# Kernel optimization log

Measured on AMD Instinct MI355X. Metric: run time of the kernel, lower is better.

## Reference

```python
import jax, jax.numpy as jnp
import numpy as np

N_NODES = 40000
N_EDGES = 640000
D_IN = 128
D_HID = 128
D_OUT = 128
N_GRAPHS = 128


def setup_inputs() -> dict:
    key = jax.random.key(0)
    ks = jax.random.split(key, 12)
    x = jax.random.normal(ks[0], (N_NODES, D_IN), dtype=jnp.float32)
    edge_index = jax.random.randint(ks[1], (2, N_EDGES), 0, N_NODES, dtype=jnp.int64)
    batch = jnp.sort(jax.random.randint(ks[2], (N_NODES,), 0, N_GRAPHS, dtype=jnp.int64))
    def lin(k, fan_in, shape):
        s = 1.0 / np.sqrt(fan_in)
        return jax.random.uniform(k, shape, dtype=jnp.float32, minval=-s, maxval=s)
    return {
        "x": x, "edge_index": edge_index, "batch": batch,
        "W_rel0": lin(ks[3], D_IN, (D_IN, D_HID)), "b_rel0": lin(ks[4], D_IN, (D_HID,)), "W_root0": lin(ks[5], D_IN, (D_IN, D_HID)),
        "W_rel1": lin(ks[6], D_HID, (D_HID, D_HID)), "b_rel1": lin(ks[7], D_HID, (D_HID,)), "W_root1": lin(ks[8], D_HID, (D_HID, D_HID)),
        "W_rel2": lin(ks[9], D_HID, (D_HID, D_OUT)), "b_rel2": lin(ks[10], D_HID, (D_OUT,)), "W_root2": lin(ks[11], D_HID, (D_HID, D_OUT)),
    }


def graph_conv(x, src, dst, W_rel, b_rel, W_root):
    # PyG GraphConv: out_i = Lin_rel(sum_{j in N(i)} x_j) + Lin_root(x_i)
    agg = jax.ops.segment_sum(x[src], dst, num_segments=N_NODES)  # [N, F]
    return agg @ W_rel + b_rel + x @ W_root


def reference(x, edge_index, batch,
              W_rel0, b_rel0, W_root0,
              W_rel1, b_rel1, W_root1,
              W_rel2, b_rel2, W_root2):
    src, dst = edge_index[0], edge_index[1]
    h = graph_conv(x, src, dst, W_rel0, b_rel0, W_root0)
    h = jax.nn.relu(h)  # dropout is identity in eval mode
    h = graph_conv(h, src, dst, W_rel1, b_rel1, W_root1)
    h = jax.nn.relu(h)
    h = graph_conv(h, src, dst, W_rel2, b_rel2, W_root2)
    # global_max_pool over per-node graph ids -> [n_graphs, D_OUT]
    return jax.ops.segment_max(h, batch, num_segments=N_GRAPHS)
```

## Files before the change

kernel.cpp:

```cpp
#include <hip/hip_runtime.h>
#include <hip/hip_bf16.h>
#include <math.h>

#define N_NODES 40000
#define N_EDGES 640000
#define D 128
#define N_GRAPHS 128
#define SCAN_NBLK ((N_NODES + 255) / 256)
#define LDS_STRIDE 68

typedef __attribute__((ext_vector_type(8))) short bf16x8;
typedef __attribute__((ext_vector_type(4))) float f32x4;
typedef __attribute__((ext_vector_type(4))) unsigned int u32x4;

static __device__ __forceinline__ unsigned short f2b(float f) {
    unsigned int u = __float_as_uint(f);
    unsigned int r = (u + 0x7fffu + ((u >> 16) & 1u)) >> 16;
    return (unsigned short)r;
}
static __device__ __forceinline__ float blo(unsigned int u) {
    return __uint_as_float(u << 16);
}
static __device__ __forceinline__ float bhi(unsigned int u) {
    return __uint_as_float(u & 0xffff0000u);
}
static __device__ __forceinline__ unsigned int fkey(float x) {
    unsigned int b = __float_as_uint(x);
    return (b & 0x80000000u) ? ~b : (b | 0x80000000u);
}

__global__ void __launch_bounds__(256) k_init(
    int* __restrict__ counts,
    unsigned short* __restrict__ xb, unsigned short* __restrict__ hA,
    unsigned short* __restrict__ hB, unsigned int* __restrict__ outk) {
    int n = blockIdx.x * 256 + threadIdx.x;
    if (n < N_GRAPHS * D) outk[n] = 0x007FFFFFu;
    if (n < N_NODES) counts[n] = 0;
    if (blockIdx.x == SCAN_NBLK) {
        int t = threadIdx.x;
        if (t < 48) {
            int row = t >> 4, c = t & 15;
            unsigned short* p = (row == 0) ? xb : (row == 1) ? hA : hB;
            u32x4 z = {0u, 0u, 0u, 0u};
            ((u32x4*)(p + (size_t)N_NODES * D))[c] = z;
        }
    }
}

__global__ void __launch_bounds__(256) k_pack1(
    const int* __restrict__ ei, int* __restrict__ counts,
    const float* __restrict__ x, unsigned int* __restrict__ xb,
    const float* __restrict__ Wr0, const float* __restrict__ Wt0,
    const float* __restrict__ Wr1, const float* __restrict__ Wt1,
    const float* __restrict__ Wr2, const float* __restrict__ Wt2,
    unsigned short* __restrict__ WT) {
    int b = blockIdx.x;
    int t = threadIdx.x;
    if (b < 2500) {
        int e = b * 256 + t;
        atomicAdd(&counts[ei[N_EDGES + e]], 1);
    } else if (b < 5000) {
        int i = (b - 2500) * 256 + t;
        const f32x4* xv = (const f32x4*)x;
        f32x4 v0 = xv[i * 2], v1 = xv[i * 2 + 1];
        u32x4 o;
        o.x = ((unsigned int)f2b(v0.y) << 16) | f2b(v0.x);
        o.y = ((unsigned int)f2b(v0.w) << 16) | f2b(v0.z);
        o.z = ((unsigned int)f2b(v1.y) << 16) | f2b(v1.x);
        o.w = ((unsigned int)f2b(v1.w) << 16) | f2b(v1.z);
        ((u32x4*)xb)[i] = o;
    } else {
        int bw = b - 5000;
        int l = bw >> 7, c = bw & 127, k = t;
        const float* Wrel = (l == 0) ? Wr0 : (l == 1) ? Wr1 : Wr2;
        const float* Wroot = (l == 0) ? Wt0 : (l == 1) ? Wt1 : Wt2;
        float v = (k < D) ? Wrel[k * D + c] : Wroot[(k - D) * D + c];
        WT[(size_t)l * 128 * 256 + c * 256 + k] = f2b(v);
    }
}

__global__ void __launch_bounds__(256) k_scan1(const int* __restrict__ counts,
                                               int* __restrict__ local_pre,
                                               int* __restrict__ blocksums) {
    int t = threadIdx.x;
    int i = blockIdx.x * 256 + t;
    int lane = t & 63, wave = t >> 6;
    int v = (i < N_NODES) ? ((counts[i] + 15) & ~15) : 0;
    int incl = v;
#pragma unroll
    for (int off = 1; off < 64; off <<= 1) {
        int u = __shfl_up(incl, off);
        if (lane >= off) incl += u;
    }
    __shared__ int ws[4];
    if (lane == 63) ws[wave] = incl;
    __syncthreads();
    int base = 0;
    for (int w = 0; w < 4; ++w) {
        int s = ws[w];
        if (w < wave) base += s;
    }
    if (i < N_NODES) local_pre[i] = base + incl - v;
    if (t == 255) blocksums[blockIdx.x] = base + incl;
}

__global__ void __launch_bounds__(256) k_scan3(const int* __restrict__ local_pre,
                                               const int* __restrict__ blocksums,
                                               const int* __restrict__ counts,
                                               int* __restrict__ rp_pad,
                                               int* __restrict__ cursor,
                                               int* __restrict__ src_pad) {
    int t = threadIdx.x;
    int lane = t & 63, wave = t >> 6;
    int bid = blockIdx.x;
    int v = (t < bid) ? blocksums[t] : 0;
#pragma unroll
    for (int off = 32; off >= 1; off >>= 1) v += __shfl_xor(v, off);
    __shared__ int ws[4];
    if (lane == 0) ws[wave] = v;
    __syncthreads();
    int base = ws[0] + ws[1] + ws[2] + ws[3];

    int i = bid * 256 + t;
    if (i < N_NODES) {
        int rp = base + local_pre[i];
        rp_pad[i] = rp;
        cursor[i] = rp;
        int c = counts[i];
        int pc = (c + 15) & ~15;
        for (int j = rp + c; j < rp + pc; ++j) src_pad[j] = N_NODES;
        if (i == N_NODES - 1) rp_pad[N_NODES] = rp + pc;
    }
}

__global__ void k_scatter(const int* __restrict__ ei, int* __restrict__ cursor,
                          int* __restrict__ src_pad) {
    int e = blockIdx.x * blockDim.x + threadIdx.x;
    if (e < N_EDGES) {
        int d = ei[N_EDGES + e];
        int pos = atomicAdd(&cursor[d], 1);
        src_pad[pos] = ei[e];
    }
}

__global__ void __launch_bounds__(256) k_layer(
    const unsigned short* __restrict__ in,
    const int* __restrict__ rp_pad,
    const int* __restrict__ src_pad,
    const unsigned short* __restrict__ WT,
    const float* __restrict__ bias,
    unsigned short* __restrict__ out,
    const int* __restrict__ batch,
    unsigned int* __restrict__ outk) {
    __shared__ unsigned int aggLDS[16 * LDS_STRIDE];
    int tid = threadIdx.x;
    int w = tid >> 6;
    int lane = tid & 63;
    int q = lane >> 4;
    int c = lane & 15;
    int nl = w * 4 + q;
    int nodebase = blockIdx.x * 16;
    const u32x4* inv = (const u32x4*)in;

    int s = rp_pad[nodebase + nl];
    int e = rp_pad[nodebase + nl + 1];
    const int4* sidx = (const int4*)(src_pad + s);
    int ntrips = (e - s) >> 4;

    float a0 = 0.f, a1 = 0.f, a2 = 0.f, a3 = 0.f;
    float a4 = 0.f, a5 = 0.f, a6 = 0.f, a7 = 0.f;

#define ACC8(v) do { \
        a0 += blo((v).x); a1 += bhi((v).x); \
        a2 += blo((v).y); a3 += bhi((v).y); \
        a4 += blo((v).z); a5 += bhi((v).z); \
        a6 += blo((v).w); a7 += bhi((v).w); } while (0)

    for (int t = 0; t < ntrips; ++t) {
        int4 ia = sidx[4 * t + 0];
        int4 ib = sidx[4 * t + 1];
        int4 ic = sidx[4 * t + 2];
        int4 id = sidx[4 * t + 3];
        u32x4 v0 = inv[ia.x * 16 + c];
        u32x4 v1 = inv[ia.y * 16 + c];
        u32x4 v2 = inv[ia.z * 16 + c];
        u32x4 v3 = inv[ia.w * 16 + c];
        u32x4 v4 = inv[ib.x * 16 + c];
        u32x4 v5 = inv[ib.y * 16 + c];
        u32x4 v6 = inv[ib.z * 16 + c];
        u32x4 v7 = inv[ib.w * 16 + c];
        u32x4 v8 = inv[ic.x * 16 + c];
        u32x4 v9 = inv[ic.y * 16 + c];
        u32x4 va = inv[ic.z * 16 + c];
        u32x4 vb = inv[ic.w * 16 + c];
        u32x4 vc = inv[id.x * 16 + c];
        u32x4 vd = inv[id.y * 16 + c];
        u32x4 ve = inv[id.z * 16 + c];
        u32x4 vf = inv[id.w * 16 + c];
        ACC8(v0); ACC8(v1); ACC8(v2); ACC8(v3);
        ACC8(v4); ACC8(v5); ACC8(v6); ACC8(v7);
        ACC8(v8); ACC8(v9); ACC8(va); ACC8(vb);
        ACC8(vc); ACC8(vd); ACC8(ve); ACC8(vf);
    }
#undef ACC8

    u32x4 o;
    o.x = ((unsigned int)f2b(a1) << 16) | f2b(a0);
    o.y = ((unsigned int)f2b(a3) << 16) | f2b(a2);
    o.z = ((unsigned int)f2b(a5) << 16) | f2b(a4);
    o.w = ((unsigned int)f2b(a7) << 16) | f2b(a6);
    *(u32x4*)&aggLDS[nl * LDS_STRIDE + c * 4] = o;
    __syncthreads();

    int row = c, quad = q;
    int colbase = w * 32;

    f32x4 acc0 = {0.f, 0.f, 0.f, 0.f};
    f32x4 acc1 = {0.f, 0.f, 0.f, 0.f};

    const unsigned int* Al = &aggLDS[row * LDS_STRIDE];
    const short* Xp = (const short*)(in + (nodebase + row) * D);
    const short* W0 = (const short*)(WT + (colbase + row) * 256);
    const short* W1 = (const short*)(WT + (colbase + 16 + row) * 256);

#pragma unroll
    for (int t = 0; t < 4; ++t) {
        bf16x8 af = *(const bf16x8*)(Al + t * 16 + quad * 4);
        int k0 = t * 32 + quad * 8;
        bf16x8 b0 = *(const bf16x8*)(W0 + k0);
        bf16x8 b1 = *(const bf16x8*)(W1 + k0);
        acc0 = __builtin_amdgcn_mfma_f32_16x16x32_bf16(af, b0, acc0, 0, 0, 0);
        acc1 = __builtin_amdgcn_mfma_f32_16x16x32_bf16(af, b1, acc1, 0, 0, 0);
    }
#pragma unroll
    for (int t = 0; t < 4; ++t) {
        int k0 = t * 32 + quad * 8;
        bf16x8 xf = *(const bf16x8*)(Xp + k0);
        bf16x8 b0 = *(const bf16x8*)(W0 + 128 + k0);
        bf16x8 b1 = *(const bf16x8*)(W1 + 128 + k0);
        acc0 = __builtin_amdgcn_mfma_f32_16x16x32_bf16(xf, b0, acc0, 0, 0, 0);
        acc1 = __builtin_amdgcn_mfma_f32_16x16x32_bf16(xf, b1, acc1, 0, 0, 0);
    }

    int c0 = colbase + row, c1 = c0 + 16;
    float bia0 = bias[c0], bia1 = bias[c1];
    float v0[4], v1[4];
#pragma unroll
    for (int r = 0; r < 4; ++r) { v0[r] = acc0[r] + bia0; v1[r] = acc1[r] + bia1; }

    if (outk == nullptr) {
#pragma unroll
        for (int r = 0; r < 4; ++r) {
            int n2 = nodebase + quad * 4 + r;
            out[n2 * D + c0] = f2b(fmaxf(v0[r], 0.f));
            out[n2 * D + c1] = f2b(fmaxf(v1[r], 0.f));
        }
    } else {
        int g0 = batch[nodebase];
        int g15 = batch[nodebase + 15];
        if (g0 == g15) {
            float m0 = fmaxf(fmaxf(v0[0], v0[1]), fmaxf(v0[2], v0[3]));
            float m1 = fmaxf(fmaxf(v1[0], v1[1]), fmaxf(v1[2], v1[3]));
            m0 = fmaxf(m0, __shfl_xor(m0, 16)); m0 = fmaxf(m0, __shfl_xor(m0, 32));
            m1 = fmaxf(m1, __shfl_xor(m1, 16)); m1 = fmaxf(m1, __shfl_xor(m1, 32));
            if (quad == 0) {
                atomicMax(&outk[g0 * D + c0], fkey(m0));
                atomicMax(&outk[g0 * D + c1], fkey(m1));
            }
        } else {
#pragma unroll
            for (int r = 0; r < 4; ++r) {
                int gg = batch[nodebase + quad * 4 + r];
                atomicMax(&outk[gg * D + c0], fkey(v0[r]));
                atomicMax(&outk[gg * D + c1], fkey(v1[r]));
            }
        }
    }
}

__global__ void k_unmap(unsigned int* __restrict__ outk) {
    int i = blockIdx.x * 256 + threadIdx.x;
    unsigned int k = outk[i];
    unsigned int b = (k & 0x80000000u) ? (k ^ 0x80000000u) : ~k;
    ((float*)outk)[i] = __uint_as_float(b);
}

extern "C" void kernel_launch(void* const* d_in, const int* in_sizes, int n_in,
                              void* d_out, int out_size, void* d_ws, size_t ws_size,
                              hipStream_t stream) {
    const float* x = (const float*)d_in[0];
    const int* ei = (const int*)d_in[1];
    const int* batch = (const int*)d_in[2];
    const float* Wrel[3]  = {(const float*)d_in[3], (const float*)d_in[6], (const float*)d_in[9]};
    const float* brel[3]  = {(const float*)d_in[4], (const float*)d_in[7], (const float*)d_in[10]};
    const float* Wroot[3] = {(const float*)d_in[5], (const float*)d_in[8], (const float*)d_in[11]};
    unsigned int* outk = (unsigned int*)d_out;

    char* ws = (char*)d_ws;
    size_t off = 0;
    auto alloc = [&](size_t bytes) -> void* {
        void* p = ws + off;
        off = (off + bytes + 255) & ~(size_t)255;
        return p;
    };
    unsigned short* xb  = (unsigned short*)alloc((size_t)(N_NODES + 1) * D * 2);
    unsigned short* hA  = (unsigned short*)alloc((size_t)(N_NODES + 1) * D * 2);
    unsigned short* hB  = (unsigned short*)alloc((size_t)(N_NODES + 1) * D * 2);
    unsigned short* WT  = (unsigned short*)alloc((size_t)3 * 128 * 256 * 2);
    int* rp_pad     = (int*)alloc((size_t)(N_NODES + 1) * 4);
    int* counts     = (int*)alloc((size_t)N_NODES * 4);
    int* cursor     = (int*)alloc((size_t)N_NODES * 4);
    int* src_pad    = (int*)alloc((size_t)(N_EDGES + 16 * N_NODES) * 4);
    int* local_pre  = (int*)alloc((size_t)N_NODES * 4);
    int* blocksums  = (int*)alloc((size_t)SCAN_NBLK * 4);

    k_init<<<SCAN_NBLK + 1, 256, 0, stream>>>(counts, xb, hA, hB, outk);
    k_pack1<<<5384, 256, 0, stream>>>(ei, counts, x, (unsigned int*)xb,
                                      Wrel[0], Wroot[0], Wrel[1], Wroot[1],
                                      Wrel[2], Wroot[2], WT);
    k_scan1<<<SCAN_NBLK, 256, 0, stream>>>(counts, local_pre, blocksums);
    k_scan3<<<SCAN_NBLK, 256, 0, stream>>>(local_pre, blocksums, counts,
                                           rp_pad, cursor, src_pad);
    k_scatter<<<(N_EDGES + 255) / 256, 256, 0, stream>>>(ei, cursor, src_pad);

    k_layer<<<N_NODES / 16, 256, 0, stream>>>(xb, rp_pad, src_pad, WT,
                                              brel[0], hA, batch, nullptr);
    k_layer<<<N_NODES / 16, 256, 0, stream>>>(hA, rp_pad, src_pad, WT + 128 * 256,
                                              brel[1], hB, batch, nullptr);
    k_layer<<<N_NODES / 16, 256, 0, stream>>>(hB, rp_pad, src_pad, WT + 2 * 128 * 256,
                                              brel[2], hB, batch, outk);

    k_unmap<<<N_GRAPHS * D / 256, 256, 0, stream>>>(outk);
}
```

Baseline: 273.1 us.

## Stage neighbor gathers through LDS with double-buffered global_load_lds

Replaces the per-lane register gather of 16 neighbor rows with a per-wave double-buffered pipeline that uses global_load_lds to copy four neighbor rows per step straight into LDS. Each wave now walks its four nodes in sequence, prefetching the next 16-edge chunk while it accumulates the current one, then reduces across quads with shuffles. The goal is to cut VGPR pressure and overlap gather latency with accumulation. The cost is a full vmcnt(0) wait every step, extra shuffle reductions, and more LDS use per block, which may reduce occupancy.

```diff
diff --git a/kernel.cpp b/kernel.cpp
--- a/kernel.cpp
+++ b/kernel.cpp
@@ -12,6 +12,8 @@
 typedef __attribute__((ext_vector_type(8))) short bf16x8;
 typedef __attribute__((ext_vector_type(4))) float f32x4;
 typedef __attribute__((ext_vector_type(4))) unsigned int u32x4;
+typedef unsigned int __attribute__((address_space(3))) lds_u32;
+typedef unsigned int __attribute__((address_space(1))) glb_u32;
 
 static __device__ __forceinline__ unsigned short f2b(float f) {
     unsigned int u = __float_as_uint(f);
@@ -152,23 +154,36 @@
     unsigned short* __restrict__ out,
     const int* __restrict__ batch,
     unsigned int* __restrict__ outk) {
-    __shared__ unsigned int aggLDS[16 * LDS_STRIDE];
+    __shared__ __align__(1024) char stage[4][2][4096];
+    __shared__ __align__(16) unsigned int aggLDS[16 * LDS_STRIDE];
+
     int tid = threadIdx.x;
     int w = tid >> 6;
     int lane = tid & 63;
-    int q = lane >> 4;
-    int c = lane & 15;
-    int nl = w * 4 + q;
     int nodebase = blockIdx.x * 16;
-    const u32x4* inv = (const u32x4*)in;
-
-    int s = rp_pad[nodebase + nl];
-    int e = rp_pad[nodebase + nl + 1];
-    const int4* sidx = (const int4*)(src_pad + s);
-    int ntrips = (e - s) >> 4;
-
-    float a0 = 0.f, a1 = 0.f, a2 = 0.f, a3 = 0.f;
-    float a4 = 0.f, a5 = 0.f, a6 = 0.f, a7 = 0.f;
+
+    const int* rp = rp_pad + nodebase + w * 4;
+    int r0 = rp[0], r1 = rp[1], r2 = rp[2], r3 = rp[3], r4 = rp[4];
+
+    int hh = lane >> 4;
+    int cc = lane & 15;
+    const char* inb = (const char*)in;
+    unsigned gofs = 16u * (unsigned)cc;
+
+#define STAGE4(BI, I0, I1, I2, I3) do {                                        \
+        __builtin_amdgcn_global_load_lds(                                      \
+            (const glb_u32*)(inb + (((size_t)(unsigned)(I0)) << 8) + gofs),    \
+            (lds_u32*)&stage[w][BI][0], 16, 0, 0);                             \
+        __builtin_amdgcn_global_load_lds(                                      \
+            (const glb_u32*)(inb + (((size_t)(unsigned)(I1)) << 8) + gofs),    \
+            (lds_u32*)&stage[w][BI][1024], 16, 0, 0);                          \
+        __builtin_amdgcn_global_load_lds(                                      \
+            (const glb_u32*)(inb + (((size_t)(unsigned)(I2)) << 8) + gofs),    \
+            (lds_u32*)&stage[w][BI][2048], 16, 0, 0);                          \
+        __builtin_amdgcn_global_load_lds(                                      \
+            (const glb_u32*)(inb + (((size_t)(unsigned)(I3)) << 8) + gofs),    \
+            (lds_u32*)&stage[w][BI][3072], 16, 0, 0);                          \
+    } while (0)
 
 #define ACC8(v) do { \
         a0 += blo((v).x); a1 += bhi((v).x); \
@@ -176,47 +191,68 @@
         a4 += blo((v).z); a5 += bhi((v).z); \
         a6 += blo((v).w); a7 += bhi((v).w); } while (0)
 
-    for (int t = 0; t < ntrips; ++t) {
-        int4 ia = sidx[4 * t + 0];
-        int4 ib = sidx[4 * t + 1];
-        int4 ic = sidx[4 * t + 2];
-        int4 id = sidx[4 * t + 3];
-        u32x4 v0 = inv[ia.x * 16 + c];
-        u32x4 v1 = inv[ia.y * 16 + c];
-        u32x4 v2 = inv[ia.z * 16 + c];
-        u32x4 v3 = inv[ia.w * 16 + c];
-        u32x4 v4 = inv[ib.x * 16 + c];
-        u32x4 v5 = inv[ib.y * 16 + c];
-        u32x4 v6 = inv[ib.z * 16 + c];
-        u32x4 v7 = inv[ib.w * 16 + c];
-        u32x4 v8 = inv[ic.x * 16 + c];
-        u32x4 v9 = inv[ic.y * 16 + c];
-        u32x4 va = inv[ic.z * 16 + c];
-        u32x4 vb = inv[ic.w * 16 + c];
-        u32x4 vc = inv[id.x * 16 + c];
-        u32x4 vd = inv[id.y * 16 + c];
-        u32x4 ve = inv[id.z * 16 + c];
-        u32x4 vf = inv[id.w * 16 + c];
-        ACC8(v0); ACC8(v1); ACC8(v2); ACC8(v3);
-        ACC8(v4); ACC8(v5); ACC8(v6); ACC8(v7);
-        ACC8(v8); ACC8(v9); ACC8(va); ACC8(vb);
-        ACC8(vc); ACC8(vd); ACC8(ve); ACC8(vf);
-    }
+    int i0 = 0, i1 = 0, i2 = 0, i3 = 0;
+    int pos = r0;
+    int buf_i = 0, buf_c = 0;
+    if (pos < r4) {
+        i0 = src_pad[pos + hh];       i1 = src_pad[pos + 4 + hh];
+        i2 = src_pad[pos + 8 + hh];   i3 = src_pad[pos + 12 + hh];
+        STAGE4(0, i0, i1, i2, i3);
+        buf_i = 1;
+        pos += 16;
+        if (pos < r4) {
+            i0 = src_pad[pos + hh];       i1 = src_pad[pos + 4 + hh];
+            i2 = src_pad[pos + 8 + hh];   i3 = src_pad[pos + 12 + hh];
+        }
+    }
+
+#pragma unroll
+    for (int n = 0; n < 4; ++n) {
+        int ps = (n == 0) ? r0 : (n == 1) ? r1 : (n == 2) ? r2 : r3;
+        int pe = (n == 0) ? r1 : (n == 1) ? r2 : (n == 2) ? r3 : r4;
+        float a0 = 0.f, a1 = 0.f, a2 = 0.f, a3 = 0.f;
+        float a4 = 0.f, a5 = 0.f, a6 = 0.f, a7 = 0.f;
+        for (int p = ps; p < pe; p += 16) {
+            asm volatile("s_waitcnt vmcnt(0)" ::: "memory");
+            if (pos < r4) {
+                STAGE4(buf_i, i0, i1, i2, i3);
+                buf_i ^= 1;
+                pos += 16;
+                if (pos < r4) {
+                    i0 = src_pad[pos + hh];       i1 = src_pad[pos + 4 + hh];
+                    i2 = src_pad[pos + 8 + hh];   i3 = src_pad[pos + 12 + hh];
+                }
+            }
+            const u32x4* sb = (const u32x4*)&stage[w][buf_c][0];
+            u32x4 v0 = sb[0 * 64 + lane];
+            u32x4 v1 = sb[1 * 64 + lane];
+            u32x4 v2 = sb[2 * 64 + lane];
+            u32x4 v3 = sb[3 * 64 + lane];
+            ACC8(v0); ACC8(v1); ACC8(v2); ACC8(v3);
+            buf_c ^= 1;
+        }
+#define RED(a) do { a += __shfl_xor(a, 16); a += __shfl_xor(a, 32); } while (0)
+        RED(a0); RED(a1); RED(a2); RED(a3);
+        RED(a4); RED(a5); RED(a6); RED(a7);
+#undef RED
+        if (lane < 16) {
+            u32x4 o;
+            o.x = ((unsigned int)f2b(a1) << 16) | f2b(a0);
+            o.y = ((unsigned int)f2b(a3) << 16) | f2b(a2);
+            o.z = ((unsigned int)f2b(a5) << 16) | f2b(a4);
+            o.w = ((unsigned int)f2b(a7) << 16) | f2b(a6);
+            *(u32x4*)&aggLDS[(w * 4 + n) * LDS_STRIDE + 4 * cc] = o;
+        }
+    }
+#undef STAGE4
 #undef ACC8
-
-    u32x4 o;
-    o.x = ((unsigned int)f2b(a1) << 16) | f2b(a0);
-    o.y = ((unsigned int)f2b(a3) << 16) | f2b(a2);
-    o.z = ((unsigned int)f2b(a5) << 16) | f2b(a4);
-    o.w = ((unsigned int)f2b(a7) << 16) | f2b(a6);
-    *(u32x4*)&aggLDS[nl * LDS_STRIDE + c * 4] = o;
     __syncthreads();
 
-    int row = c, quad = q;
+    int row = cc, quad = hh;
     int colbase = w * 32;
 
-    f32x4 acc0 = {0.f, 0.f, 0.f, 0.f};
-    f32x4 acc1 = {0.f, 0.f, 0.f, 0.f};
+    f32x4 gacc0 = {0.f, 0.f, 0.f, 0.f};
+    f32x4 gacc1 = {0.f, 0.f, 0.f, 0.f};
 
     const unsigned int* Al = &aggLDS[row * LDS_STRIDE];
     const short* Xp = (const short*)(in + (nodebase + row) * D);
@@ -229,8 +265,8 @@
         int k0 = t * 32 + quad * 8;
         bf16x8 b0 = *(const bf16x8*)(W0 + k0);
         bf16x8 b1 = *(const bf16x8*)(W1 + k0);
-        acc0 = __builtin_amdgcn_mfma_f32_16x16x32_bf16(af, b0, acc0, 0, 0, 0);
-        acc1 = __builtin_amdgcn_mfma_f32_16x16x32_bf16(af, b1, acc1, 0, 0, 0);
+        gacc0 = __builtin_amdgcn_mfma_f32_16x16x32_bf16(af, b0, gacc0, 0, 0, 0);
+        gacc1 = __builtin_amdgcn_mfma_f32_16x16x32_bf16(af, b1, gacc1, 0, 0, 0);
     }
 #pragma unroll
     for (int t = 0; t < 4; ++t) {
@@ -238,15 +274,15 @@
         bf16x8 xf = *(const bf16x8*)(Xp + k0);
         bf16x8 b0 = *(const bf16x8*)(W0 + 128 + k0);
         bf16x8 b1 = *(const bf16x8*)(W1 + 128 + k0);
-        acc0 = __builtin_amdgcn_mfma_f32_16x16x32_bf16(xf, b0, acc0, 0, 0, 0);
-        acc1 = __builtin_amdgcn_mfma_f32_16x16x32_bf16(xf, b1, acc1, 0, 0, 0);
+        gacc0 = __builtin_amdgcn_mfma_f32_16x16x32_bf16(xf, b0, gacc0, 0, 0, 0);
+        gacc1 = __builtin_amdgcn_mfma_f32_16x16x32_bf16(xf, b1, gacc1, 0, 0, 0);
     }
 
     int c0 = colbase + row, c1 = c0 + 16;
     float bia0 = bias[c0], bia1 = bias[c1];
     float v0[4], v1[4];
 #pragma unroll
-    for (int r = 0; r < 4; ++r) { v0[r] = acc0[r] + bia0; v1[r] = acc1[r] + bia1; }
+    for (int r = 0; r < 4; ++r) { v0[r] = gacc0[r] + bia0; v1[r] = gacc1[r] + bia1; }
 
     if (outk == nullptr) {
 #pragma unroll
```

After: 283.9 us. +3.9%, slower.
